# Kernel optimization log

Hardware: AMD Instinct MI355X
Metric: run time of the kernel (lower is better)

Reference implementation:

```python
import jax, jax.numpy as jnp
import numpy as np

EPS = 1e-6


def _greedy_kcenter_select(cosine, k):
    """Greedy diversity selection (k-center) exactly matching SLAMFormer.Pruner.

    cosine: [L, L] distance matrix (1 - cosine similarity).
    k: static Python int, number of tokens to keep.
    Returns sorted int32 indices of shape [k].
    """
    # torch.topk(cosine, 2, dim=0, largest=False).values[1]: second-smallest per column.
    two_smallest = -jax.lax.top_k(-cosine.T, 2)[0]  # [L, 2], ascending per column
    initial_scores = two_smallest[:, 1]              # [L]
    first = jnp.argmax(initial_scores)
    scores0 = cosine[first].at[first].set(-jnp.inf)  # running min-distance to selected set

    def step(scores, _):
        idx = jnp.argmax(scores)
        scores = jnp.minimum(scores, cosine[idx]).at[idx].set(-jnp.inf)
        return scores, idx

    _, rest = jax.lax.scan(step, scores0, None, length=k - 1)
    sel = jnp.concatenate([first[None], rest])
    return jnp.sort(sel)


def setup_inputs() -> dict:
    key = jax.random.key(0)
    L, C = 4096, 1024  # patch tokens per frame x decoder dim (dinov2-large decoder)
    x = jax.random.normal(key, (L, C), dtype=jnp.float32)
    return {
        "visual_feature_vectors": x,
        "image_feature_length": L,
        "threshold_terms": 1024,  # round(0.25 * L), DivPrune default ratio
    }


def reference(visual_feature_vectors, image_feature_length, threshold_terms):
    x = visual_feature_vectors
    # pairwise_cosine_similarity with clamp_min(1e-6) on the row norms
    norm = jnp.maximum(jnp.linalg.norm(x, axis=1, keepdims=True), EPS)
    xn = x / norm
    cosine = 1.0 - xn @ xn.T  # [L, L] distance matrix
    k = max(1, min(int(threshold_terms), int(image_feature_length)))
    sel = _greedy_kcenter_select(cosine, k)
    return sel, cosine
```

## Files before the change

kernel.cpp:

```cpp
#include <hip/hip_runtime.h>
#include <math.h>

__global__ void rownorm_kernel(const float* __restrict__ x,
                               float* __restrict__ rnorm, int C) {
    int row = blockIdx.x;
    const float4* xr = (const float4*)(x + (size_t)row * C);
    int n4 = C >> 2;
    float s = 0.f;
    for (int c = threadIdx.x; c < n4; c += blockDim.x) {
        float4 v = xr[c];
        s += v.x * v.x + v.y * v.y + v.z * v.z + v.w * v.w;
    }
    for (int off = 32; off > 0; off >>= 1) s += __shfl_down(s, off, 64);
    __shared__ float red[4];
    int lane = threadIdx.x & 63, wid = threadIdx.x >> 6;
    if (lane == 0) red[wid] = s;
    __syncthreads();
    if (threadIdx.x == 0) {
        float t = red[0] + red[1] + red[2] + red[3];
        float n = fmaxf(sqrtf(t), 1e-6f);
        rnorm[row] = 1.0f / n;
    }
}

#define BM 128
#define BN 128
#define BK 32

__global__ __launch_bounds__(256) void cosine_gemm(
        const float* __restrict__ x, const float* __restrict__ rnorm,
        float* __restrict__ cosine, int L, int C) {
    if (blockIdx.x < blockIdx.y) return;
    __shared__ float As[BK][BM + 4];
    __shared__ float Bs[BK][BN + 4];
    const int tid = threadIdx.x;
    const int i0 = blockIdx.y * BM;
    const int j0 = blockIdx.x * BN;
    const int tr = (tid >> 4) << 3;
    const int tc = (tid & 15) << 3;
    const int lr = tid >> 3;
    const int lc = (tid & 7) << 2;
    float acc[8][8] = {};

    for (int k0 = 0; k0 < C; k0 += BK) {
#pragma unroll
        for (int q = 0; q < 4; ++q) {
            int r = lr + q * 32;
            float ra = rnorm[i0 + r];
            float4 va = *(const float4*)(x + (size_t)(i0 + r) * C + k0 + lc);
            As[lc + 0][r] = va.x * ra;
            As[lc + 1][r] = va.y * ra;
            As[lc + 2][r] = va.z * ra;
            As[lc + 3][r] = va.w * ra;
            float rb = rnorm[j0 + r];
            float4 vb = *(const float4*)(x + (size_t)(j0 + r) * C + k0 + lc);
            Bs[lc + 0][r] = vb.x * rb;
            Bs[lc + 1][r] = vb.y * rb;
            Bs[lc + 2][r] = vb.z * rb;
            Bs[lc + 3][r] = vb.w * rb;
        }
        __syncthreads();
#pragma unroll
        for (int kk = 0; kk < BK; ++kk) {
            float a[8], b[8];
#pragma unroll
            for (int m = 0; m < 8; ++m) a[m] = As[kk][tr + m];
#pragma unroll
            for (int n = 0; n < 8; ++n) b[n] = Bs[kk][tc + n];
#pragma unroll
            for (int m = 0; m < 8; ++m)
#pragma unroll
                for (int n = 0; n < 8; ++n)
                    acc[m][n] = fmaf(a[m], b[n], acc[m][n]);
        }
        __syncthreads();
    }
#pragma unroll
    for (int m = 0; m < 8; ++m) {
        float* crow = cosine + (size_t)(i0 + tr + m) * L + j0 + tc;
        float4 o0 = {1.f - acc[m][0], 1.f - acc[m][1], 1.f - acc[m][2], 1.f - acc[m][3]};
        float4 o1 = {1.f - acc[m][4], 1.f - acc[m][5], 1.f - acc[m][6], 1.f - acc[m][7]};
        ((float4*)crow)[0] = o0;
        ((float4*)crow)[1] = o1;
    }
    if (i0 != j0) {
#pragma unroll
        for (int n = 0; n < 8; ++n) {
            float* trow = cosine + (size_t)(j0 + tc + n) * L + i0 + tr;
            float4 t0 = {1.f - acc[0][n], 1.f - acc[1][n], 1.f - acc[2][n], 1.f - acc[3][n]};
            float4 t1 = {1.f - acc[4][n], 1.f - acc[5][n], 1.f - acc[6][n], 1.f - acc[7][n]};
            ((float4*)trow)[0] = t0;
            ((float4*)trow)[1] = t1;
        }
    }
}

__global__ void twosmallest_kernel(const float* __restrict__ cosine,
                                   float* __restrict__ min2, int L) {
    int row = blockIdx.x;
    const float4* r4 = (const float4*)(cosine + (size_t)row * L);
    float4 v0 = r4[threadIdx.x];
    float4 v1 = r4[threadIdx.x + 256];
    float4 v2 = r4[threadIdx.x + 512];
    float4 v3 = r4[threadIdx.x + 768];

#define PAIR_INIT(M1, M2, V)                                   \
    float M1 = fminf(V.x, V.y), M2 = fmaxf(V.x, V.y);          \
    { float _n1 = fminf(M1, V.z); M2 = fminf(M2, fmaxf(M1, V.z)); M1 = _n1; \
      _n1 = fminf(M1, V.w); M2 = fminf(M2, fmaxf(M1, V.w)); M1 = _n1; }
    PAIR_INIT(a1, a2, v0)
    PAIR_INIT(b1, b2, v1)
    PAIR_INIT(c1, c2, v2)
    PAIR_INIT(d1, d2, v3)
#undef PAIR_INIT
    float m1 = fminf(a1, b1), m2 = fminf(fmaxf(a1, b1), fminf(a2, b2));
    float n1 = fminf(c1, d1), n2 = fminf(fmaxf(c1, d1), fminf(c2, d2));
    float m1r = fminf(m1, n1), m2r = fminf(fmaxf(m1, n1), fminf(m2, n2));

    for (int off = 32; off > 0; off >>= 1) {
        float om1 = __shfl_down(m1r, off, 64);
        float om2 = __shfl_down(m2r, off, 64);
        float nm1 = fminf(m1r, om1);
        float nm2 = fminf(fmaxf(m1r, om1), fminf(m2r, om2));
        m1r = nm1; m2r = nm2;
    }
    __shared__ float s1[4], s2[4];
    int lane = threadIdx.x & 63, wid = threadIdx.x >> 6;
    if (lane == 0) { s1[wid] = m1r; s2[wid] = m2r; }
    __syncthreads();
    if (threadIdx.x == 0) {
        float x1 = s1[0], x2 = s2[0];
        for (int w = 1; w < 4; ++w) {
            float y1 = s1[w], y2 = s2[w];
            float z2 = fminf(fmaxf(x1, y1), fminf(x2, y2));
            x1 = fminf(x1, y1);
            x2 = z2;
        }
        min2[row] = x2;
    }
}

#define FOR16(X) X(0) X(1) X(2) X(3) X(4) X(5) X(6) X(7) \
                 X(8) X(9) X(10) X(11) X(12) X(13) X(14) X(15)

#define ARGMAX16(BV, BJ)                                                      \
  do {                                                                        \
    float _t0,_t1,_t2,_t3,_t4,_t5,_t6,_t7;                                    \
    int _u0,_u1,_u2,_u3,_u4,_u5,_u6,_u7;                                      \
    bool _g;                                                                  \
    _g = sc1  > sc0;  _t0 = _g ? sc1  : sc0;  _u0 = _g ? base+1  : base+0;    \
    _g = sc3  > sc2;  _t1 = _g ? sc3  : sc2;  _u1 = _g ? base+3  : base+2;    \
    _g = sc5  > sc4;  _t2 = _g ? sc5  : sc4;  _u2 = _g ? base+5  : base+4;    \
    _g = sc7  > sc6;  _t3 = _g ? sc7  : sc6;  _u3 = _g ? base+7  : base+6;    \
    _g = sc9  > sc8;  _t4 = _g ? sc9  : sc8;  _u4 = _g ? base+9  : base+8;    \
    _g = sc11 > sc10; _t5 = _g ? sc11 : sc10; _u5 = _g ? base+11 : base+10;   \
    _g = sc13 > sc12; _t6 = _g ? sc13 : sc12; _u6 = _g ? base+13 : base+12;   \
    _g = sc15 > sc14; _t7 = _g ? sc15 : sc14; _u7 = _g ? base+15 : base+14;   \
    _g = _t1 > _t0; _t0 = _g ? _t1 : _t0; _u0 = _g ? _u1 : _u0;               \
    _g = _t3 > _t2; _t2 = _g ? _t3 : _t2; _u2 = _g ? _u3 : _u2;               \
    _g = _t5 > _t4; _t4 = _g ? _t5 : _t4; _u4 = _g ? _u5 : _u4;               \
    _g = _t7 > _t6; _t6 = _g ? _t7 : _t6; _u6 = _g ? _u7 : _u6;               \
    _g = _t2 > _t0; _t0 = _g ? _t2 : _t0; _u0 = _g ? _u2 : _u0;               \
    _g = _t6 > _t4; _t4 = _g ? _t6 : _t4; _u4 = _g ? _u6 : _u4;               \
    _g = _t4 > _t0; BV = _g ? _t4 : _t0; BJ = _g ? _u4 : _u0;                 \
  } while (0)

#define DPP_FMAX(V, CTRL)                                                     \
  do {                                                                        \
    int _b = __builtin_amdgcn_update_dpp(                                     \
        __float_as_int(V), __float_as_int(V), (CTRL), 0xf, 0xf, false);       \
    (V) = fmaxf((V), __int_as_float(_b));                                     \
  } while (0)

#define BAR_NOVM()                                                \
  do {                                                            \
    asm volatile("s_waitcnt lgkmcnt(0)" ::: "memory");            \
    __builtin_amdgcn_s_barrier();                                 \
    asm volatile("" ::: "memory");                                \
  } while (0)

static __device__ __forceinline__ void wave_argmax(float bv, int bj,
                                                   float& wv, int& wj) {
    float v = bv;
    DPP_FMAX(v, 0x111);
    DPP_FMAX(v, 0x112);
    DPP_FMAX(v, 0x114);
    DPP_FMAX(v, 0x118);
    DPP_FMAX(v, 0x142);
    DPP_FMAX(v, 0x143);
    float wmax = __int_as_float(
        __builtin_amdgcn_readlane(__float_as_int(v), 63));
    unsigned long long m = __ballot(bv == wmax);
    int lowlane = __ffsll((unsigned long long)m) - 1;
    wj = __builtin_amdgcn_readlane(bj, lowlane);
    wv = wmax;
}

#define GSTEP(PIN0,PIN1,PIN2,PIN3, PREDIN, POUT0,POUT1,POUT2,POUT3, PREDOUT)  \
  {                                                                           \
    float wv_; int wj_;                                                       \
    wave_argmax(bv, bj, wv_, wj_);                                            \
    if (lane == 0) { sv[p][wid] = wv_; si[p][wid] = wj_; }                    \
    BAR_NOVM();                                                               \
    float4 cv4 = *(const float4*)&sv[p][0];                                   \
    int4 ci4 = *(const int4*)&si[p][0];                                       \
    p ^= 1;                                                                   \
    float cwv = cv4.x; int wi_ = ci4.x; int wsl = 0;                          \
    if (cv4.y > cwv) { cwv = cv4.y; wi_ = ci4.y; wsl = 1; }                   \
    if (cv4.z > cwv) { cwv = cv4.z; wi_ = ci4.z; wsl = 2; }                   \
    if (cv4.w > cwv) { cwv = cv4.w; wi_ = ci4.w; wsl = 3; }                   \
    int wiu = __builtin_amdgcn_readfirstlane(wi_);                            \
    float e0 = (wsl == 0) ? -INFINITY : cv4.x;                                \
    float e1 = (wsl == 1) ? -INFINITY : cv4.y;                                \
    float e2 = (wsl == 2) ? -INFINITY : cv4.z;                                \
    float e3 = (wsl == 3) ? -INFINITY : cv4.w;                                \
    float rv = e0; int ri_ = ci4.x;                                           \
    if (e1 > rv) { rv = e1; ri_ = ci4.y; }                                    \
    if (e2 > rv) { rv = e2; ri_ = ci4.z; }                                    \
    if (e3 > rv) { rv = e3; ri_ = ci4.w; }                                    \
    int riu = __builtin_amdgcn_readfirstlane(ri_);                            \
      \
                           \
    float4 q0, q1, q2, q3;                                                    \
    if (wiu == PREDIN) {                                                      \
        q0 = PIN0; q1 = PIN1; q2 = PIN2; q3 = PIN3;                           \
    } else {                                                                  \
        const float4* rp_ = (const float4*)(cosine + (size_t)wiu * L) + (tid<<2); \
        q0 = rp_[0]; q1 = rp_[1]; q2 = rp_[2]; q3 = rp_[3];                   \
    }                                                                         \
    __builtin_amdgcn_sched_barrier(0);                                        \
     \
    const float4* sp_ = (const float4*)(cosine + (size_t)riu * L) + (tid<<2); \
    POUT0 = sp_[0]; POUT1 = sp_[1]; POUT2 = sp_[2]; POUT3 = sp_[3];           \
    PREDOUT = riu;                                                            \
    __builtin_amdgcn_sched_barrier(0);                                        \
    int sl = ((wiu >> 4) == tid) ? (wiu & 15) : -1;                           \
    sc0  = (sl == 0)  ? -INFINITY : fminf(sc0, q0.x);                         \
    sc1  = (sl == 1)  ? -INFINITY : fminf(sc1, q0.y);                         \
    sc2  = (sl == 2)  ? -INFINITY : fminf(sc2, q0.z);                         \
    sc3  = (sl == 3)  ? -INFINITY : fminf(sc3, q0.w);                         \
    sc4  = (sl == 4)  ? -INFINITY : fminf(sc4, q1.x);                         \
    sc5  = (sl == 5)  ? -INFINITY : fminf(sc5, q1.y);                         \
    sc6  = (sl == 6)  ? -INFINITY : fminf(sc6, q1.z);                         \
    sc7  = (sl == 7)  ? -INFINITY : fminf(sc7, q1.w);                         \
    sc8  = (sl == 8)  ? -INFINITY : fminf(sc8, q2.x);                         \
    sc9  = (sl == 9)  ? -INFINITY : fminf(sc9, q2.y);                         \
    sc10 = (sl == 10) ? -INFINITY : fminf(sc10, q2.z);                        \
    sc11 = (sl == 11) ? -INFINITY : fminf(sc11, q2.w);                        \
    sc12 = (sl == 12) ? -INFINITY : fminf(sc12, q3.x);                        \
    sc13 = (sl == 13) ? -INFINITY : fminf(sc13, q3.y);                        \
    sc14 = (sl == 14) ? -INFINITY : fminf(sc14, q3.z);                        \
    sc15 = (sl == 15) ? -INFINITY : fminf(sc15, q3.w);                        \
    ARGMAX16(bv, bj);                                                         \
  }

__global__ __launch_bounds__(256) void greedy_kernel(
        const float* __restrict__ cosine, const float* __restrict__ min2,
        float* __restrict__ sel_out, int L, int k) {
    const int tid = threadIdx.x;
    const int lane = tid & 63, wid = tid >> 6;
    __shared__ __align__(16) float sv[2][4];
    __shared__ __align__(16) int si[2][4];
    __shared__ int wsum[4];
    const int base = tid << 4;

#define DECL_SC(i) float sc##i;
    FOR16(DECL_SC)

    float bv; int bj;

    {
        const float4* m4 = (const float4*)min2 + (tid << 2);
        float4 q0 = m4[0], q1 = m4[1], q2 = m4[2], q3 = m4[3];
        sc0 = q0.x;  sc1 = q0.y;  sc2 = q0.z;  sc3 = q0.w;
        sc4 = q1.x;  sc5 = q1.y;  sc6 = q1.z;  sc7 = q1.w;
        sc8 = q2.x;  sc9 = q2.y;  sc10 = q2.z; sc11 = q2.w;
        sc12 = q3.x; sc13 = q3.y; sc14 = q3.z; sc15 = q3.w;
    }
    ARGMAX16(bv, bj);
    {
        float wv; int wj;
        wave_argmax(bv, bj, wv, wj);
        if (lane == 0) { sv[0][wid] = wv; si[0][wid] = wj; }
    }
    __syncthreads();
    int first;
    {
        float4 cv4 = *(const float4*)&sv[0][0];
        int4 ci4 = *(const int4*)&si[0][0];
        float wv = cv4.x; int wi = ci4.x;
        if (cv4.y > wv) { wv = cv4.y; wi = ci4.y; }
        if (cv4.z > wv) { wv = cv4.z; wi = ci4.z; }
        if (cv4.w > wv) { wv = cv4.w; wi = ci4.w; }
        first = __builtin_amdgcn_readfirstlane(wi);
    }
    {
        const float4* rp = (const float4*)(cosine + (size_t)first * L) + (tid << 2);
        float4 q0 = rp[0], q1 = rp[1], q2 = rp[2], q3 = rp[3];
        int sl = ((first >> 4) == tid) ? (first & 15) : -1;
        sc0  = (sl == 0)  ? -INFINITY : q0.x;
        sc1  = (sl == 1)  ? -INFINITY : q0.y;
        sc2  = (sl == 2)  ? -INFINITY : q0.z;
        sc3  = (sl == 3)  ? -INFINITY : q0.w;
        sc4  = (sl == 4)  ? -INFINITY : q1.x;
        sc5  = (sl == 5)  ? -INFINITY : q1.y;
        sc6  = (sl == 6)  ? -INFINITY : q1.z;
        sc7  = (sl == 7)  ? -INFINITY : q1.w;
        sc8  = (sl == 8)  ? -INFINITY : q2.x;
        sc9  = (sl == 9)  ? -INFINITY : q2.y;
        sc10 = (sl == 10) ? -INFINITY : q2.z;
        sc11 = (sl == 11) ? -INFINITY : q2.w;
        sc12 = (sl == 12) ? -INFINITY : q3.x;
        sc13 = (sl == 13) ? -INFINITY : q3.y;
        sc14 = (sl == 14) ? -INFINITY : q3.z;
        sc15 = (sl == 15) ? -INFINITY : q3.w;
    }
    ARGMAX16(bv, bj);

    int p = 1;
    int predA = -1, predB = -1;
    float4 a0 = {0,0,0,0}, a1 = {0,0,0,0}, a2 = {0,0,0,0}, a3 = {0,0,0,0};
    float4 b0 = {0,0,0,0}, b1 = {0,0,0,0}, b2 = {0,0,0,0}, b3 = {0,0,0,0};
    int it = 0;
    for (; it + 1 < k - 1; it += 2) {
        GSTEP(a0,a1,a2,a3, predA, b0,b1,b2,b3, predB)
        GSTEP(b0,b1,b2,b3, predB, a0,a1,a2,a3, predA)
    }
    if (it < k - 1) {
        GSTEP(a0,a1,a2,a3, predA, b0,b1,b2,b3, predB)
    }
    asm volatile("" :: "v"(b0.x), "v"(b1.x), "v"(b2.x), "v"(b3.x),
                       "v"(a0.x), "v"(a1.x), "v"(a2.x), "v"(a3.x));

    unsigned flags = 0; int cnt = 0;
#define FLAGBIT(i) if (sc##i == -INFINITY) { flags |= (1u << i); ++cnt; }
    FOR16(FLAGBIT)
    int incl = cnt;
#pragma unroll
    for (int off = 1; off < 64; off <<= 1) {
        int n = __shfl_up(incl, off, 64);
        if (lane >= off) incl += n;
    }
    if (lane == 63) wsum[wid] = incl;
    __syncthreads();
    int off0 = 0;
#pragma unroll
    for (int w = 0; w < 4; ++w)
        if (w < wid) off0 += wsum[w];
    int pos = off0 + incl - cnt;
#pragma unroll
    for (int j = 0; j < 16; ++j)
        if ((flags >> j) & 1) sel_out[pos++] = (float)(base + j);
}

extern "C" void kernel_launch(void* const* d_in, const int* in_sizes, int n_in,
                              void* d_out, int out_size, void* d_ws, size_t ws_size,
                              hipStream_t stream) {
    const float* x = (const float*)d_in[0];

    long long L = (long long)floor(sqrt((double)out_size));
    while (L * L > (long long)out_size) --L;
    while ((L + 1) * (L + 1) <= (long long)out_size) ++L;
    long long k = (long long)out_size - L * L;
    long long C = (long long)in_sizes[0] / L;

    float* sel = (float*)d_out;
    float* cosine = (float*)d_out + k;
    float* rnorm = (float*)d_ws;
    float* min2 = rnorm + L;

    rownorm_kernel<<<(int)L, 256, 0, stream>>>(x, rnorm, (int)C);
    dim3 g2((int)(L / BN), (int)(L / BM));
    cosine_gemm<<<g2, 256, 0, stream>>>(x, rnorm, cosine, (int)L, (int)C);
    twosmallest_kernel<<<(int)L, 256, 0, stream>>>(cosine, min2, (int)L);
    greedy_kernel<<<1, 256, 0, stream>>>(cosine, min2, sel, (int)L, (int)k);
}
```

Before: 1.176 ms.

## Launch only upper-triangle GEMM tiles and prefetch next K-slice into registers

```diff
diff --git a/kernel.cpp b/kernel.cpp
--- a/kernel.cpp
+++ b/kernel.cpp
@@ -30,36 +30,60 @@
 __global__ __launch_bounds__(256) void cosine_gemm(
         const float* __restrict__ x, const float* __restrict__ rnorm,
         float* __restrict__ cosine, int L, int C) {
-    if (blockIdx.x < blockIdx.y) return;
+    int t = blockIdx.x;
+    int r = (int)((sqrtf(8.f * t + 1.f) - 1.f) * 0.5f);
+    while (r * (r + 1) / 2 > t) --r;
+    while ((r + 1) * (r + 2) / 2 <= t) ++r;
+    int bx = r, by = t - r * (r + 1) / 2;
+
     __shared__ float As[BK][BM + 4];
     __shared__ float Bs[BK][BN + 4];
     const int tid = threadIdx.x;
-    const int i0 = blockIdx.y * BM;
-    const int j0 = blockIdx.x * BN;
+    const int i0 = by * BM;
+    const int j0 = bx * BN;
     const int tr = (tid >> 4) << 3;
     const int tc = (tid & 15) << 3;
     const int lr = tid >> 3;
     const int lc = (tid & 7) << 2;
     float acc[8][8] = {};
 
-    for (int k0 = 0; k0 < C; k0 += BK) {
+    float raq[4], rbq[4];
+#pragma unroll
+    for (int q = 0; q < 4; ++q) {
+        raq[q] = rnorm[i0 + lr + q * 32];
+        rbq[q] = rnorm[j0 + lr + q * 32];
+    }
+
+    float4 va[4], vb[4];
+#pragma unroll
+    for (int q = 0; q < 4; ++q) {
+        va[q] = *(const float4*)(x + (size_t)(i0 + lr + q * 32) * C + lc);
+        vb[q] = *(const float4*)(x + (size_t)(j0 + lr + q * 32) * C + lc);
+    }
+
+    const int nt = C / BK;
+    for (int kt = 0; kt < nt; ++kt) {
 #pragma unroll
         for (int q = 0; q < 4; ++q) {
-            int r = lr + q * 32;
-            float ra = rnorm[i0 + r];
-            float4 va = *(const float4*)(x + (size_t)(i0 + r) * C + k0 + lc);
-            As[lc + 0][r] = va.x * ra;
-            As[lc + 1][r] = va.y * ra;
-            As[lc + 2][r] = va.z * ra;
-            As[lc + 3][r] = va.w * ra;
-            float rb = rnorm[j0 + r];
-            float4 vb = *(const float4*)(x + (size_t)(j0 + r) * C + k0 + lc);
-            Bs[lc + 0][r] = vb.x * rb;
-            Bs[lc + 1][r] = vb.y * rb;
-            Bs[lc + 2][r] = vb.z * rb;
-            Bs[lc + 3][r] = vb.w * rb;
+            int rr = lr + q * 32;
+            As[lc + 0][rr] = va[q].x * raq[q];
+            As[lc + 1][rr] = va[q].y * raq[q];
+            As[lc + 2][rr] = va[q].z * raq[q];
+            As[lc + 3][rr] = va[q].w * raq[q];
+            Bs[lc + 0][rr] = vb[q].x * rbq[q];
+            Bs[lc + 1][rr] = vb[q].y * rbq[q];
+            Bs[lc + 2][rr] = vb[q].z * rbq[q];
+            Bs[lc + 3][rr] = vb[q].w * rbq[q];
         }
         __syncthreads();
+        if (kt + 1 < nt) {
+            int k0 = (kt + 1) * BK;
+#pragma unroll
+            for (int q = 0; q < 4; ++q) {
+                va[q] = *(const float4*)(x + (size_t)(i0 + lr + q * 32) * C + k0 + lc);
+                vb[q] = *(const float4*)(x + (size_t)(j0 + lr + q * 32) * C + k0 + lc);
+            }
+        }
 #pragma unroll
         for (int kk = 0; kk < BK; ++kk) {
             float a[8], b[8];
@@ -370,8 +394,9 @@
     float* min2 = rnorm + L;
 
     rownorm_kernel<<<(int)L, 256, 0, stream>>>(x, rnorm, (int)C);
-    dim3 g2((int)(L / BN), (int)(L / BM));
-    cosine_gemm<<<g2, 256, 0, stream>>>(x, rnorm, cosine, (int)L, (int)C);
+    int nb = (int)(L / BM);
+    int ntri = nb * (nb + 1) / 2;
+    cosine_gemm<<<ntri, 256, 0, stream>>>(x, rnorm, cosine, (int)L, (int)C);
     twosmallest_kernel<<<(int)L, 256, 0, stream>>>(cosine, min2, (int)L);
     greedy_kernel<<<1, 256, 0, stream>>>(cosine, min2, sel, (int)L, (int)k);
 }
```

After: 1.250 ms. 6.2% more time.
